# Performance work log

Hardware: AMD Instinct MI355X
Metric: run time of the kernel (lower is better)

The kernel has to match this reference:

```python
import jax, jax.numpy as jnp
import numpy as np

N = 65536      # num drones/nodes
E = 262144     # num directed edges
HID = 128      # hidden_dim
HEADS = 8      # gat1 heads
EPS = 1e-5


def _bn(x, g, b):
    # BatchNorm1d in training mode: batch statistics over dim 0 (biased var)
    mu = x.mean(0)
    var = ((x - mu) ** 2).mean(0)
    return (x - mu) * jax.lax.rsqrt(var + EPS) * g + b


def _gat(x, src, dst, W, a_src, a_dst, bias, heads, out_c, n, concat):
    # PyG GATConv math (self-loops already included in src/dst)
    xw = (x @ W).reshape(n, heads, out_c)               # [N,H,C]
    al_s = (xw * a_src).sum(-1)                          # [N,H]
    al_d = (xw * a_dst).sum(-1)                          # [N,H]
    e = jax.nn.leaky_relu(al_s[src] + al_d[dst], 0.2)    # [E',H]
    m = jax.ops.segment_max(e, dst, num_segments=n)      # stable softmax per target
    ex = jnp.exp(e - m[dst])
    den = jax.ops.segment_sum(ex, dst, num_segments=n)
    alpha = ex / den[dst]                                # [E',H]
    out = jax.ops.segment_sum(xw[src] * alpha[:, :, None], dst, num_segments=n)
    out = out.reshape(n, heads * out_c) if concat else out.mean(axis=1)
    return out + bias


def setup_inputs() -> dict:
    key = jax.random.key(0)
    ks = jax.random.split(key, 24)
    s = 0.05
    inp = {
        'node_features': jax.random.normal(ks[0], (N, HID), jnp.float32),
        'relative_poses': jax.random.normal(ks[1], (E, 6), jnp.float32),
        'pe_w1': jax.random.normal(ks[2], (6, 64), jnp.float32) * s,
        'pe_b1': jnp.zeros((64,), jnp.float32),
        'pe_g1': jnp.ones((64,), jnp.float32),
        'pe_be1': jnp.zeros((64,), jnp.float32),
        'pe_w2': jax.random.normal(ks[3], (64, HID), jnp.float32) * s,
        'pe_b2': jnp.zeros((HID,), jnp.float32),
        'pe_g2': jnp.ones((HID,), jnp.float32),
        'pe_be2': jnp.zeros((HID,), jnp.float32),
        'gamma_w': jax.random.normal(ks[4], (HID, HID), jnp.float32) * s,
        'gamma_b': jnp.zeros((HID,), jnp.float32),
        'beta_w': jax.random.normal(ks[5], (HID, HID), jnp.float32) * s,
        'beta_b': jnp.zeros((HID,), jnp.float32),
        'g1_w': jax.random.normal(ks[6], (HID, HEADS * HID), jnp.float32) * s,
        'g1_as': jax.random.normal(ks[7], (HEADS, HID), jnp.float32) * s,
        'g1_ad': jax.random.normal(ks[8], (HEADS, HID), jnp.float32) * s,
        'g1_b': jnp.zeros((HEADS * HID,), jnp.float32),
        'g2_w': jax.random.normal(ks[9], (HEADS * HID, HID), jnp.float32) * s,
        'g2_as': jax.random.normal(ks[10], (1, HID), jnp.float32) * s,
        'g2_ad': jax.random.normal(ks[11], (1, HID), jnp.float32) * s,
        'g2_b': jnp.zeros((HID,), jnp.float32),
        'edge_index': jax.random.randint(ks[12], (2, E), 0, N, jnp.int32),
    }
    return inp


def reference(node_features, relative_poses, pe_w1, pe_b1, pe_g1, pe_be1,
              pe_w2, pe_b2, pe_g2, pe_be2, gamma_w, gamma_b, beta_w, beta_b,
              g1_w, g1_as, g1_ad, g1_b, g2_w, g2_as, g2_ad, g2_b, edge_index):
    src, dst = edge_index[0], edge_index[1]
    # SpatialEncoding: pose MLP with training-mode BN, then FiLM modulation
    h = jax.nn.relu(_bn(relative_poses @ pe_w1 + pe_b1, pe_g1, pe_be1))
    h = jax.nn.relu(_bn(h @ pe_w2 + pe_b2, pe_g2, pe_be2))
    gamma = jax.nn.sigmoid(h @ gamma_w + gamma_b) * 2.0   # [E,HID]
    beta = h @ beta_w + beta_b
    modulated = gamma * node_features[src] + beta          # [E,HID]
    last = jnp.full((N,), -1, jnp.int32).at[dst].max(jnp.arange(E, dtype=jnp.int32))
    enc = jnp.where((last >= 0)[:, None], modulated[jnp.clip(last, 0)], node_features)
    # add self loops (PyG GATConv default)
    loops = jnp.arange(N, dtype=src.dtype)
    src_a = jnp.concatenate([src, loops])
    dst_a = jnp.concatenate([dst, loops])
    x = jax.nn.elu(_gat(enc, src_a, dst_a, g1_w, g1_as, g1_ad, g1_b, HEADS, HID, N, True))
    # dropout is identity in eval mode
    out = _gat(x, src_a, dst_a, g2_w, g2_as, g2_ad, g2_b, 1, HID, N, False)
    return out
```

## Files before the change

kernel.cpp:

```cpp
#include <hip/hip_runtime.h>
#include <hip/hip_bf16.h>
#include <math.h>

#define NN 65536
#define EE 262144

typedef unsigned short u16;
typedef unsigned int u32;
typedef __attribute__((ext_vector_type(8))) short bf16x8;
typedef __attribute__((ext_vector_type(4))) float f32x4;

__device__ __forceinline__ float bfu2f(u16 u){ return __uint_as_float(((u32)u)<<16); }
__device__ __forceinline__ u16 f2bfu(float f){
  u32 x = __float_as_uint(f);
  return (u16)((x + 0x7fffu + ((x>>16)&1u)) >> 16);
}
__device__ __forceinline__ float lrelu(float x){ return x>0.f ? x : 0.2f*x; }
__device__ __forceinline__ float fexp(float x){ return __expf(x); }

__global__ void k_prep(const float* __restrict__ nodef, u16* __restrict__ nodefb,
                       const float* __restrict__ pe_w2, u16* __restrict__ pe_w2t,
                       const float* __restrict__ gamma_w, u16* __restrict__ gwt,
                       const float* __restrict__ beta_w, u16* __restrict__ bwt,
                       const float* __restrict__ g1_w, u16* __restrict__ g1wt,
                       const float* __restrict__ g2_w, u16* __restrict__ g2wt,
                       const float* __restrict__ g1_as, const float* __restrict__ g1_ad,
                       u16* __restrict__ vtb,
                       const int* __restrict__ dstA, int* __restrict__ lastE, int* __restrict__ deg){
  int bid = blockIdx.x, t = threadIdx.x;
  if (bid < 8192){
    int i = (bid*256+t)*4;
    float4 v = *(const float4*)(nodef + i);
    ushort4 o; o.x=f2bfu(v.x); o.y=f2bfu(v.y); o.z=f2bfu(v.z); o.w=f2bfu(v.w);
    *(ushort4*)(nodefb + i) = o;
  } else if (bid < 8224){
    int idx = (bid-8192)*256+t;
    int k = idx>>7, n = idx&127;
    pe_w2t[n*64+k] = f2bfu(pe_w2[idx]);
  } else if (bid < 8288){
    int idx = (bid-8224)*256+t;
    int k = idx>>7, n = idx&127;
    gwt[n*128+k] = f2bfu(gamma_w[idx]);
  } else if (bid < 8352){
    int idx = (bid-8288)*256+t;
    int k = idx>>7, n = idx&127;
    bwt[n*128+k] = f2bfu(beta_w[idx]);
  } else if (bid < 8864){
    int idx = (bid-8352)*256+t;
    int k = idx>>10, n = idx&1023;
    g1wt[n*128+k] = f2bfu(g1_w[idx]);
  } else if (bid < 9376){
    int idx = (bid-8864)*256+t;
    int k = idx>>7, n = idx&127;
    g2wt[n*1024+k] = f2bfu(g2_w[idx]);
  } else if (bid < 9380){
    int gid = (bid-9376)*256+t;
    if (gid<1024){
      int h = gid>>7, k = gid&127;
      float s=0.f,d=0.f;
      for (int cc=0;cc<128;++cc){
        float wv = g1_w[(size_t)k*1024 + h*128+cc];
        s=fmaf(wv,g1_as[h*128+cc],s); d=fmaf(wv,g1_ad[h*128+cc],d);
      }
      vtb[h*128+k] = f2bfu(s);
      vtb[(h+8)*128+k] = f2bfu(d);
    }
  } else {
    int e = (bid-9380)*256+t;
    int d = dstA[e];
    atomicMax(&lastE[d], e);
    atomicAdd(&deg[d], 1);
  }
}

__launch_bounds__(256)
__global__ void k_bn1p(const float* __restrict__ poses, const float* __restrict__ w1,
                       const float* __restrict__ b1, float* __restrict__ part1){
  int t = threadIdx.x;
  int wv = t>>6, c = t&63;
  int wave = blockIdx.x*4 + wv;
  float wc[6];
#pragma unroll
  for (int j=0;j<6;++j) wc[j] = w1[j*64+c];
  float bb = b1[c];
  float s=0.f,q=0.f;
  int e0 = wave*(EE/1024);
  for (int e=e0;e<e0+(EE/1024);++e){
    float z = bb;
#pragma unroll
    for (int j=0;j<6;++j) z = fmaf(poses[e*6+j], wc[j], z);
    s += z; q += z*z;
  }
  __shared__ float ls[4][64];
  __shared__ float lq[4][64];
  ls[wv][c]=s; lq[wv][c]=q;
  __syncthreads();
  if (t<64){
    float ss = ls[0][t]+ls[1][t]+ls[2][t]+ls[3][t];
    float qq = lq[0][t]+lq[1][t]+lq[2][t]+lq[3][t];
    part1[blockIdx.x*128 + t] = ss;
    part1[blockIdx.x*128 + 64 + t] = qq;
  }
}

__global__ void k_bn_fin1(const float* __restrict__ part1,
                          const float* __restrict__ g, const float* __restrict__ be,
                          float* __restrict__ a, float* __restrict__ cc){
  int c = threadIdx.x;
  if (c<64){
    float s=0.f,q=0.f;
    for (int k=0;k<256;++k){ s += part1[k*128+c]; q += part1[k*128+64+c]; }
    float mu = s*(1.f/EE);
    float var = q*(1.f/EE) - mu*mu;
    float istd = rsqrtf(var + 1e-5f);
    float ac = istd*g[c];
    a[c] = ac;
    cc[c] = be[c] - mu*ac;
  }
}

__global__ void k_red2(const float* __restrict__ psum, const float* __restrict__ psq,
                       float* __restrict__ part2){
  int t = threadIdx.x;
  int b0 = blockIdx.x*128;
  float s = 0.f;
  if (t < 128){
    for (int k=0;k<128;++k) s += psum[(size_t)(b0+k)*128 + t];
  } else {
    int c = t-128;
    for (int k=0;k<128;++k) s += psq[(size_t)(b0+k)*128 + c];
  }
  part2[blockIdx.x*256 + t] = s;
}

__global__ void k_bn_fin2(const float* __restrict__ part2,
                          const float* __restrict__ g, const float* __restrict__ be,
                          const float* __restrict__ bias0,
                          float* __restrict__ a, float* __restrict__ cc){
  int c = threadIdx.x;
  if (c<128){
    float s=0.f,q=0.f;
    for (int k=0;k<32;++k){ s += part2[k*256+c]; q += part2[k*256+128+c]; }
    float mu = s*(1.f/EE);
    float var = q*(1.f/EE) - mu*mu;
    float istd = rsqrtf(var + 1e-5f);
    float ac = istd*g[c];
    a[c] = ac;
    cc[c] = be[c] - mu*ac + bias0[c]*ac;
  }
}

__global__ void k_h1(const float* __restrict__ poses, const float* __restrict__ w1, const float* __restrict__ b1,
                     const float* __restrict__ a1, const float* __restrict__ c1, u16* __restrict__ h1){
  int idx = blockIdx.x*256+threadIdx.x;
  int e = idx>>5, cp = (idx&31)*2;
  float z0 = b1[cp], z1 = b1[cp+1];
#pragma unroll
  for (int j=0;j<6;++j){
    float pv = poses[e*6+j];
    z0 = fmaf(pv, w1[j*64+cp], z0);
    z1 = fmaf(pv, w1[j*64+cp+1], z1);
  }
  float h0 = z0*a1[cp]+c1[cp];     h0 = h0>0.f?h0:0.f;
  float h1v = z1*a1[cp+1]+c1[cp+1]; h1v = h1v>0.f?h1v:0.f;
  *(u32*)(h1 + (size_t)e*64 + cp) = (u32)f2bfu(h0) | ((u32)f2bfu(h1v)<<16);
}

template<int EPI>
__launch_bounds__(256)
__global__ void k_mm(const u16* __restrict__ A, const u16* __restrict__ Bt,
                     const u16* __restrict__ Bt2,
                     int K, int lda, int ldbt, int ldc,
                     u16* __restrict__ outb,
                     const float* __restrict__ bias, const float* __restrict__ bias2,
                     float* __restrict__ ssum, float* __restrict__ ssq,
                     const float* __restrict__ gb,
                     const float* __restrict__ bb, const u16* __restrict__ nfselb,
                     const int* __restrict__ lastE){
  const int m0 = blockIdx.x*64, n0 = blockIdx.y*128;
  const int t = threadIdx.x;
  const int lane = t & 63, wv = t>>6;
  const int wr = wv>>1, wc = wv&1;
  __shared__ u16 Als[64*64];
  __shared__ u16 Bls[128*64];
  __shared__ u16 B2ls[EPI==7 ? 128*64 : 8];
  __shared__ float epiS[128][2];
  __shared__ float epiD[128][2];
  f32x4 acc[2][4];
  f32x4 acc2[2][4];
#pragma unroll
  for (int i=0;i<2;++i)
#pragma unroll
    for (int j=0;j<4;++j){ acc[i][j] = (f32x4){0.f,0.f,0.f,0.f}; acc2[i][j] = (f32x4){0.f,0.f,0.f,0.f}; }

  for (int k0=0;k0<K;k0+=64){
    constexpr int NS = (EPI==7) ? 10 : 6;
#pragma unroll
    for (int c=0;c<NS;++c){
      int gc = c*256 + t;
      if (gc < 512){
        int row = gc>>3, ch = gc&7;
        int sw = ((row<<3)|ch) ^ (row&7);
        *(uint4*)(Als + sw*8) = *(const uint4*)(A + (size_t)(m0+row)*lda + k0 + ch*8);
      } else if (gc < 1536){
        int g2 = gc - 512;
        int row = g2>>3, ch = g2&7;
        int sw = ((row<<3)|ch) ^ (row&7);
        *(uint4*)(Bls + sw*8) = *(const uint4*)(Bt + (size_t)(n0+row)*ldbt + k0 + ch*8);
      } else if constexpr (EPI==7){
        int g2 = gc - 1536;
        int row = g2>>3, ch = g2&7;
        int sw = ((row<<3)|ch) ^ (row&7);
        *(uint4*)(B2ls + sw*8) = *(const uint4*)(Bt2 + (size_t)(n0+row)*ldbt + k0 + ch*8);
      }
    }
    __syncthreads();
#pragma unroll
    for (int kk=0;kk<2;++kk){
      bf16x8 af[2], bfr[4];
      int ch = kk*4 + (lane>>4);
#pragma unroll
      for (int i=0;i<2;++i){
        int row = wr*32 + i*16 + (lane&15);
        int sw = ((row<<3)|ch) ^ (row&7);
        af[i] = *(const bf16x8*)(Als + sw*8);
      }
#pragma unroll
      for (int j=0;j<4;++j){
        int rowb = wc*64 + j*16 + (lane&15);
        int swb = ((rowb<<3)|ch) ^ (rowb&7);
        bfr[j] = *(const bf16x8*)(Bls + swb*8);
      }
#pragma unroll
      for (int i=0;i<2;++i)
#pragma unroll
        for (int j=0;j<4;++j)
          acc[i][j] = __builtin_amdgcn_mfma_f32_16x16x32_bf16(af[i], bfr[j], acc[i][j], 0,0,0);
      if constexpr (EPI==7){
        bf16x8 bf2[4];
#pragma unroll
        for (int j=0;j<4;++j){
          int rowb = wc*64 + j*16 + (lane&15);
          int swb = ((rowb<<3)|ch) ^ (rowb&7);
          bf2[j] = *(const bf16x8*)(B2ls + swb*8);
        }
#pragma unroll
        for (int i=0;i<2;++i)
#pragma unroll
          for (int j=0;j<4;++j)
            acc2[i][j] = __builtin_amdgcn_mfma_f32_16x16x32_bf16(af[i], bf2[j], acc2[i][j], 0,0,0);
      }
    }
    __syncthreads();
  }

  int cbase = wc*64 + (lane&15);

  if constexpr (EPI==6){
    float av[4], cv[4];
#pragma unroll
    for (int j=0;j<4;++j){ av[j]=bias[cbase+j*16]; cv[j]=bias2[cbase+j*16]; }
#pragma unroll
    for (int i=0;i<2;++i)
#pragma unroll
      for (int r=0;r<4;++r){
        int row = m0 + wr*32 + i*16 + ((lane>>4)<<2) + r;
#pragma unroll
        for (int j=0;j<4;++j){
          float h = fmaf(acc[i][j][r], av[j], cv[j]);
          outb[(size_t)row*128 + cbase + j*16] = f2bfu(h>0.f?h:0.f);
        }
      }
  } else if constexpr (EPI==2){
    float bv[4];
#pragma unroll
    for (int j=0;j<4;++j) bv[j]=bias[cbase+j*16];
    float s[4]={0,0,0,0}, q[4]={0,0,0,0};
#pragma unroll
    for (int i=0;i<2;++i)
#pragma unroll
      for (int j=0;j<4;++j)
#pragma unroll
        for (int r=0;r<4;++r){ float z = acc[i][j][r]+bv[j]; s[j]+=z; q[j]+=z*z; }
#pragma unroll
    for (int j=0;j<4;++j){
      float ss=s[j], qq=q[j];
      ss += __shfl_xor(ss,16); ss += __shfl_xor(ss,32);
      qq += __shfl_xor(qq,16); qq += __shfl_xor(qq,32);
      if (lane<16){
        epiS[wc*64+j*16+lane][wr] = ss;
        epiD[wc*64+j*16+lane][wr] = qq;
      }
    }
    __syncthreads();
    if (t<128){
      ssum[(size_t)blockIdx.x*128 + t] = epiS[t][0]+epiS[t][1];
      ssq[(size_t)blockIdx.x*128 + t]  = epiD[t][0]+epiD[t][1];
    }
  } else if constexpr (EPI==7){
    float gbv[4], bbv[4];
#pragma unroll
    for (int j=0;j<4;++j){ gbv[j]=gb[cbase+j*16]; bbv[j]=bb[cbase+j*16]; }
#pragma unroll
    for (int i=0;i<2;++i)
#pragma unroll
      for (int r=0;r<4;++r){
        int n = m0 + wr*32 + i*16 + ((lane>>4)<<2) + r;
        int le = lastE[n];
#pragma unroll
        for (int j=0;j<4;++j){
          int c = cbase + j*16;
          float nv = bfu2f(nfselb[(size_t)n*128+c]);
          float res;
          if (le>=0){
            float gp = acc[i][j][r] + gbv[j];
            float gam = 2.f/(1.f+fexp(-gp));
            res = fmaf(gam, nv, acc2[i][j][r] + bbv[j]);
          } else res = nv;
          outb[(size_t)n*128+c] = f2bfu(res);
        }
      }
  }
}

__launch_bounds__(512)
__global__ void k_proj(const u16* __restrict__ aggH, const u16* __restrict__ g1wt,
                       const u16* __restrict__ g2wt, const float* __restrict__ g1b,
                       const float* __restrict__ asv, const float* __restrict__ adv,
                       u16* __restrict__ xw2b, float* __restrict__ als2, float* __restrict__ ald2){
  const int m0 = blockIdx.x*64;
  const int t = threadIdx.x, lane = t&63, wv = t>>6;
  const int wr = wv>>1, wc = wv&1;
  __shared__ u16 ATls[64*128];
  __shared__ u16 Wls[128*64];
  __shared__ float epiS[64][2];
  __shared__ float epiD[64][2];
  const int cbase = wc*64 + (lane&15);
  f32x4 acc2[4];
#pragma unroll
  for (int j=0;j<4;++j) acc2[j] = (f32x4){0.f,0.f,0.f,0.f};

  for (int hh=0; hh<8; ++hh){
    f32x4 acc1[4];
#pragma unroll
    for (int j=0;j<4;++j) acc1[j] = (f32x4){0.f,0.f,0.f,0.f};

    for (int k0=0;k0<128;k0+=64){
#pragma unroll
      for (int c=0;c<3;++c){
        int gc = c*512 + t;
        if (gc < 512){
          int row = gc>>3, ch = gc&7;
          int sw = ((row<<3)|ch) ^ (row&7);
          *(uint4*)(ATls + sw*8) = *(const uint4*)(aggH + (size_t)(m0+row)*1024 + hh*128 + k0 + ch*8);
        } else {
          int g2 = gc - 512;
          int row = g2>>3, ch = g2&7;
          int sw = ((row<<3)|ch) ^ (row&7);
          *(uint4*)(Wls + sw*8) = *(const uint4*)(g1wt + (size_t)(hh*128+row)*128 + k0 + ch*8);
        }
      }
      __syncthreads();
      __builtin_amdgcn_s_setprio(1);
#pragma unroll
      for (int kk=0;kk<2;++kk){
        bf16x8 af, bfr[4];
        int ch = kk*4 + (lane>>4);
        {
          int row = wr*16 + (lane&15);
          int sw = ((row<<3)|ch) ^ (row&7);
          af = *(const bf16x8*)(ATls + sw*8);
        }
#pragma unroll
        for (int j=0;j<4;++j){
          int rowb = wc*64 + j*16 + (lane&15);
          int swb = ((rowb<<3)|ch) ^ (rowb&7);
          bfr[j] = *(const bf16x8*)(Wls + swb*8);
        }
#pragma unroll
        for (int j=0;j<4;++j)
          acc1[j] = __builtin_amdgcn_mfma_f32_16x16x32_bf16(af, bfr[j], acc1[j], 0,0,0);
      }
      __builtin_amdgcn_s_setprio(0);
      __syncthreads();
    }
    {
      float bv[4];
#pragma unroll
      for (int j=0;j<4;++j) bv[j] = g1b[hh*128 + cbase + j*16];
#pragma unroll
      for (int r=0;r<4;++r){
        int mrow = wr*16 + ((lane>>4)<<2) + r;
#pragma unroll
        for (int j=0;j<4;++j){
          int c = cbase + j*16;
          float v = acc1[j][r] + bv[j];
          v = v>0.f ? v : fexp(v)-1.f;
          int sw = ((mrow<<4)|(c>>3)) ^ (mrow&7);
          ATls[sw*8 + (c&7)] = f2bfu(v);
        }
      }
    }
    for (int k0=0;k0<128;k0+=64){
#pragma unroll
      for (int c=0;c<2;++c){
        int g2 = c*512 + t;
        int row = g2>>3, ch = g2&7;
        int sw = ((row<<3)|ch) ^ (row&7);
        *(uint4*)(Wls + sw*8) = *(const uint4*)(g2wt + (size_t)row*1024 + hh*128 + k0 + ch*8);
      }
      __syncthreads();
      __builtin_amdgcn_s_setprio(1);
#pragma unroll
      for (int kk=0;kk<2;++kk){
        bf16x8 af, bfr[4];
        int ch = kk*4 + (lane>>4);
        int chk = (k0>>3) + ch;
        {
          int row = wr*16 + (lane&15);
          int sw = ((row<<4)|chk) ^ (row&7);
          af = *(const bf16x8*)(ATls + sw*8);
        }
#pragma unroll
        for (int j=0;j<4;++j){
          int rowb = wc*64 + j*16 + (lane&15);
          int swb = ((rowb<<3)|ch) ^ (rowb&7);
          bfr[j] = *(const bf16x8*)(Wls + swb*8);
        }
#pragma unroll
        for (int j=0;j<4;++j)
          acc2[j] = __builtin_amdgcn_mfma_f32_16x16x32_bf16(af, bfr[j], acc2[j], 0,0,0);
      }
      __builtin_amdgcn_s_setprio(0);
      __syncthreads();
    }
  }
  float av[4], dv[4];
#pragma unroll
  for (int j=0;j<4;++j){ av[j]=asv[cbase+j*16]; dv[j]=adv[cbase+j*16]; }
#pragma unroll
  for (int r=0;r<4;++r){
    int lr = wr*16 + ((lane>>4)<<2) + r;
    int row = m0 + lr;
    float s=0.f, d=0.f;
#pragma unroll
    for (int j=0;j<4;++j){
      float v = acc2[j][r];
      xw2b[(size_t)row*128 + cbase + j*16] = f2bfu(v);
      s = fmaf(v, av[j], s); d = fmaf(v, dv[j], d);
    }
#pragma unroll
    for (int o=1;o<16;o<<=1){ s += __shfl_xor(s,o); d += __shfl_xor(d,o); }
    if ((lane&15)==0){ epiS[lr][wc]=s; epiD[lr][wc]=d; }
  }
  __syncthreads();
  if (t<64){
    als2[m0+t] = epiS[t][0]+epiS[t][1];
    ald2[m0+t] = epiD[t][0]+epiD[t][1];
  }
}

__global__ void k_blocksum(const int* __restrict__ deg, int* __restrict__ bsum){
  __shared__ int s[256];
  int t = threadIdx.x;
  s[t] = deg[blockIdx.x*256+t];
  __syncthreads();
  for (int o=128;o>0;o>>=1){ if (t<o) s[t]+=s[t+o]; __syncthreads(); }
  if (!t) bsum[blockIdx.x]=s[0];
}
__global__ void k_scanb(int* __restrict__ bsum){
  __shared__ int s[256];
  int t=threadIdx.x;
  s[t]=bsum[t]; __syncthreads();
  for (int o=1;o<256;o<<=1){
    int v = s[t];
    if (t>=o) v += s[t-o];
    __syncthreads(); s[t]=v; __syncthreads();
  }
  bsum[t] = t ? s[t-1] : 0;
}
__global__ void k_indptr(const int* __restrict__ deg, const int* __restrict__ bsum, int* __restrict__ indptr){
  __shared__ int s[256];
  int t=threadIdx.x; int g=blockIdx.x*256+t;
  int d = deg[g];
  s[t]=d; __syncthreads();
  for (int o=1;o<256;o<<=1){
    int v = s[t];
    if (t>=o) v += s[t-o];
    __syncthreads(); s[t]=v; __syncthreads();
  }
  indptr[g] = bsum[blockIdx.x] + s[t] - d;
  if (g==NN-1) indptr[NN]=EE;
}
__global__ void k_fill(const int* __restrict__ srcA, const int* __restrict__ dstA,
                       const int* __restrict__ indptr, int* __restrict__ cursor, int* __restrict__ slist){
  int e = blockIdx.x*256+threadIdx.x;
  int d = dstA[e];
  int p = atomicAdd(&cursor[d],1);
  slist[indptr[d]+p] = srcA[e];
}

__global__ void k_gsel(const u16* __restrict__ h1, const u16* __restrict__ nodefb,
                       const int* __restrict__ lastE, const int* __restrict__ srcA,
                       u16* __restrict__ h1sel, u16* __restrict__ nfselb){
  int g = blockIdx.x*256+threadIdx.x;
  int n = g>>4, ch = g&15;
  int le = lastE[n];
  int src = (le>=0) ? srcA[le] : n;
  *(uint4*)(nfselb + (size_t)n*128 + ch*8) = *(const uint4*)(nodefb + (size_t)src*128 + ch*8);
  if (ch < 8){
    uint4 v = make_uint4(0,0,0,0);
    if (le>=0) v = *(const uint4*)(h1 + (size_t)le*64 + ch*8);
    *(uint4*)(h1sel + (size_t)n*64 + ch*8) = v;
  }
}

__launch_bounds__(256)
__global__ void k_als1mm(const u16* __restrict__ encb, const u16* __restrict__ vtb,
                         float* __restrict__ als, float* __restrict__ ald){
  int t = threadIdx.x, lane = t&63, wv = t>>6;
  int m0 = blockIdx.x*64 + wv*16;
  f32x4 acc = (f32x4){0.f,0.f,0.f,0.f};
  const u16* arow = encb + (size_t)(m0 + (lane&15))*128;
  const u16* brow = vtb + (lane&15)*128;
  int ko = (lane>>4)*8;
#pragma unroll
  for (int k0=0;k0<128;k0+=32){
    bf16x8 af = *(const bf16x8*)(arow + k0 + ko);
    bf16x8 bf = *(const bf16x8*)(brow + k0 + ko);
    acc = __builtin_amdgcn_mfma_f32_16x16x32_bf16(af, bf, acc, 0,0,0);
  }
  int o = lane&15;
#pragma unroll
  for (int r=0;r<4;++r){
    int row = m0 + ((lane>>4)<<2) + r;
    if (o<8) als[(size_t)row*8+o] = acc[r];
    else     ald[(size_t)row*8+(o-8)] = acc[r];
  }
}

__launch_bounds__(256)
__global__ void k_soft1(const int* __restrict__ slist, const int* __restrict__ indptr,
                        const float* __restrict__ als, const float* __restrict__ ald,
                        float* __restrict__ wcsr, float* __restrict__ den1, float* __restrict__ wself1){
  int t = threadIdx.x;
  int n = blockIdx.x*4 + (t>>6);
  int lane = t&63;
  int ei = lane>>3, h = lane&7;
  int p0 = indptr[n], p1 = indptr[n+1];
  float adh = ald[(size_t)n*8+h];
  float selfsc = lrelu(als[(size_t)n*8+h] + adh);
  float m = selfsc;
  for (int p=p0+ei; p<p1; p+=8){
    int s = slist[p];
    m = fmaxf(m, lrelu(als[(size_t)s*8+h] + adh));
  }
  m = fmaxf(m, __shfl_xor(m,8));
  m = fmaxf(m, __shfl_xor(m,16));
  m = fmaxf(m, __shfl_xor(m,32));
  float ws = fexp(selfsc - m);
  float den = (ei==0) ? ws : 0.f;
  for (int p=p0+ei; p<p1; p+=8){
    int s = slist[p];
    float w = fexp(lrelu(als[(size_t)s*8+h] + adh) - m);
    wcsr[(size_t)p*8+h] = w;
    den += w;
  }
  den += __shfl_xor(den,8);
  den += __shfl_xor(den,16);
  den += __shfl_xor(den,32);
  if (ei==0){
    den1[(size_t)n*8+h] = den;
    wself1[(size_t)n*8+h] = ws;
  }
}

__launch_bounds__(256)
__global__ void k_soft2(const int* __restrict__ slist, const int* __restrict__ indptr,
                        const float* __restrict__ als, const float* __restrict__ ald,
                        float* __restrict__ wcsr, float* __restrict__ den2, float* __restrict__ wself2){
  int t = threadIdx.x;
  int n = blockIdx.x*16 + (t>>4);
  int l = t&15;
  int p0 = indptr[n], p1 = indptr[n+1];
  float adh = ald[n];
  float selfsc = lrelu(als[n] + adh);
  float m = selfsc;
  for (int p=p0+l; p<p1; p+=16)
    m = fmaxf(m, lrelu(als[slist[p]] + adh));
  m = fmaxf(m, __shfl_xor(m,1));
  m = fmaxf(m, __shfl_xor(m,2));
  m = fmaxf(m, __shfl_xor(m,4));
  m = fmaxf(m, __shfl_xor(m,8));
  float ws = fexp(selfsc - m);
  float den = (l==0) ? ws : 0.f;
  for (int p=p0+l; p<p1; p+=16){
    float w = fexp(lrelu(als[slist[p]] + adh) - m);
    wcsr[p] = w;
    den += w;
  }
  den += __shfl_xor(den,1);
  den += __shfl_xor(den,2);
  den += __shfl_xor(den,4);
  den += __shfl_xor(den,8);
  if (l==0){ den2[n] = den; wself2[n] = ws; }
}

__launch_bounds__(256)
__global__ void k_agg1(const u16* __restrict__ encb, const float* __restrict__ wcsr,
                       const float* __restrict__ den1, const float* __restrict__ wself1,
                       const int* __restrict__ slist, const int* __restrict__ indptr,
                       u16* __restrict__ aggH){
  int t = threadIdx.x;
  int n = blockIdx.x*4 + (t>>6);
  int lane = t&63;
  int c0 = lane*2;
  int p0 = indptr[n], p1 = indptr[n+1];
  float a0[8], a1[8];
  {
    ushort2 u = *(const ushort2*)(encb + (size_t)n*128 + c0);
    float x0 = bfu2f(u.x), x1 = bfu2f(u.y);
#pragma unroll
    for (int h=0;h<8;++h){
      float ws = wself1[(size_t)n*8 + h];
      a0[h] = ws*x0; a1[h] = ws*x1;
    }
  }
  for (int p=p0; p<p1; ++p){
    int s = slist[p];
    float4 w0 = *(const float4*)(wcsr + (size_t)p*8);
    float4 w1 = *(const float4*)(wcsr + (size_t)p*8 + 4);
    ushort2 u = *(const ushort2*)(encb + (size_t)s*128 + c0);
    float x0 = bfu2f(u.x), x1 = bfu2f(u.y);
    a0[0]=fmaf(w0.x,x0,a0[0]); a1[0]=fmaf(w0.x,x1,a1[0]);
    a0[1]=fmaf(w0.y,x0,a0[1]); a1[1]=fmaf(w0.y,x1,a1[1]);
    a0[2]=fmaf(w0.z,x0,a0[2]); a1[2]=fmaf(w0.z,x1,a1[2]);
    a0[3]=fmaf(w0.w,x0,a0[3]); a1[3]=fmaf(w0.w,x1,a1[3]);
    a0[4]=fmaf(w1.x,x0,a0[4]); a1[4]=fmaf(w1.x,x1,a1[4]);
    a0[5]=fmaf(w1.y,x0,a0[5]); a1[5]=fmaf(w1.y,x1,a1[5]);
    a0[6]=fmaf(w1.z,x0,a0[6]); a1[6]=fmaf(w1.z,x1,a1[6]);
    a0[7]=fmaf(w1.w,x0,a0[7]); a1[7]=fmaf(w1.w,x1,a1[7]);
  }
#pragma unroll
  for (int h=0;h<8;++h){
    float rr = 1.f/den1[(size_t)n*8 + h];
    u32 pk = (u32)f2bfu(a0[h]*rr) | ((u32)f2bfu(a1[h]*rr)<<16);
    *(u32*)(aggH + (size_t)n*1024 + h*128 + c0) = pk;
  }
}

__launch_bounds__(256)
__global__ void k_gat2(const u16* __restrict__ xw2b, const float* __restrict__ wcsr,
                       const float* __restrict__ den2, const float* __restrict__ wself2,
                       const int* __restrict__ slist, const int* __restrict__ indptr,
                       const float* __restrict__ g2b, float* __restrict__ out){
  int t = threadIdx.x;
  int n = blockIdx.x*4 + (t>>6);
  int c0 = (t&63)*2;
  int p0 = indptr[n], p1 = indptr[n+1];
  float ws = wself2[n];
  u32 u = *(const u32*)(xw2b + (size_t)n*128 + c0);
  float a0 = ws*bfu2f((u16)u), a1 = ws*bfu2f((u16)(u>>16));
  int p = p0;
  for (; p+2<=p1; p+=2){
    int s0=slist[p], s1=slist[p+1];
    float w0=wcsr[p], w1v=wcsr[p+1];
    u32 v0 = *(const u32*)(xw2b + (size_t)s0*128 + c0);
    u32 v1 = *(const u32*)(xw2b + (size_t)s1*128 + c0);
    a0 = fmaf(w0, bfu2f((u16)v0), a0);       a1 = fmaf(w0, bfu2f((u16)(v0>>16)), a1);
    a0 = fmaf(w1v, bfu2f((u16)v1), a0);      a1 = fmaf(w1v, bfu2f((u16)(v1>>16)), a1);
  }
  for (; p<p1; ++p){
    int s = slist[p];
    float w = wcsr[p];
    u32 v = *(const u32*)(xw2b + (size_t)s*128 + c0);
    a0 = fmaf(w, bfu2f((u16)v), a0);
    a1 = fmaf(w, bfu2f((u16)(v>>16)), a1);
  }
  float rr = 1.f/den2[n];
  float2 o;
  o.x = a0*rr + g2b[c0];
  o.y = a1*rr + g2b[c0+1];
  *(float2*)(out + (size_t)n*128 + c0) = o;
}

extern "C" void kernel_launch(void* const* d_in, const int* in_sizes, int n_in,
                              void* d_out, int out_size, void* d_ws, size_t ws_size,
                              hipStream_t stream){
  const float* nodef  = (const float*)d_in[0];
  const float* poses  = (const float*)d_in[1];
  const float* pe_w1  = (const float*)d_in[2];
  const float* pe_b1  = (const float*)d_in[3];
  const float* pe_g1  = (const float*)d_in[4];
  const float* pe_be1 = (const float*)d_in[5];
  const float* pe_w2  = (const float*)d_in[6];
  const float* pe_b2  = (const float*)d_in[7];
  const float* pe_g2  = (const float*)d_in[8];
  const float* pe_be2 = (const float*)d_in[9];
  const float* gamma_w= (const float*)d_in[10];
  const float* gamma_b= (const float*)d_in[11];
  const float* beta_w = (const float*)d_in[12];
  const float* beta_b = (const float*)d_in[13];
  const float* g1_w   = (const float*)d_in[14];
  const float* g1_as  = (const float*)d_in[15];
  const float* g1_ad  = (const float*)d_in[16];
  const float* g1_b   = (const float*)d_in[17];
  const float* g2_w   = (const float*)d_in[18];
  const float* g2_as  = (const float*)d_in[19];
  const float* g2_ad  = (const float*)d_in[20];
  const float* g2_b   = (const float*)d_in[21];
  const int*   eidx   = (const int*)d_in[22];
  const int* srcA = eidx;
  const int* dstA = eidx + EE;

  char* w = (char*)d_ws;
  const size_t MB = 1048576;
  u16*   aggH  = (u16*)(w + 0);
  u16*   h1    = (u16*)(w + 0);
  u16*   h1sel = (u16*)(w + 32*MB);
  u16*   h2b   = (u16*)(w + 40*MB);
  u16*   nodefb= (u16*)(w + 56*MB);
  u16*   nfselb= (u16*)(w + 72*MB);
  float* psum  = (float*)(w + 88*MB);
  float* psq   = (float*)(w + 90*MB);
  u16*   encb  = (u16*)(w + 128*MB);
  char* sm = w + 144*MB;
  size_t off = 0;
  auto alloc = [&](size_t b)->void*{ void* p = sm+off; off += (b+255)&~(size_t)255; return p; };
  u16* pe_w2t = (u16*)alloc(64*128*2);
  u16* gwt    = (u16*)alloc(128*128*2);
  u16* bwt    = (u16*)alloc(128*128*2);
  u16* g1wt   = (u16*)alloc(1024*128*2);
  u16* g2wt   = (u16*)alloc(128*1024*2);
  u16* vtb    = (u16*)alloc(16*128*2);
  float* part2 = (float*)alloc(32*256*4);
  float* part1 = (float*)alloc(256*128*4);
  float* als1  = (float*)alloc((size_t)NN*8*4);
  float* ald1  = (float*)alloc((size_t)NN*8*4);
  float* als2  = (float*)alloc((size_t)NN*4);
  float* ald2  = (float*)alloc((size_t)NN*4);
  float* wself1= (float*)alloc((size_t)NN*8*4);
  float* den1  = (float*)alloc((size_t)NN*8*4);
  float* wcsr1 = (float*)alloc((size_t)EE*8*4);
  float* wself2= (float*)alloc((size_t)NN*4);
  float* den2  = (float*)alloc((size_t)NN*4);
  float* wcsr2 = (float*)alloc((size_t)EE*4);
  u16*  xw2b   = (u16*)alloc((size_t)NN*128*2);
  int* lastE   = (int*)alloc((size_t)NN*4);
  int* deg     = (int*)alloc((size_t)NN*4);
  int* cursor  = (int*)alloc((size_t)NN*4);
  int* indptr  = (int*)alloc((size_t)(NN+1)*4);
  int* slist   = (int*)alloc((size_t)EE*4);
  int* bsum    = (int*)alloc(1024);
  float* stats = (float*)alloc(4096);
  float* a1 = stats+384, *c1 = stats+448, *a2 = stats+512, *c2 = stats+640;

  hipMemsetAsync(deg, 0, (size_t)NN*4, stream);
  hipMemsetAsync(cursor, 0, (size_t)NN*4, stream);
  hipMemsetAsync(lastE, 0xFF, (size_t)NN*4, stream);

  k_prep<<<10404,256,0,stream>>>(nodef, nodefb, pe_w2, pe_w2t, gamma_w, gwt, beta_w, bwt,
                                 g1_w, g1wt, g2_w, g2wt, g1_as, g1_ad, vtb,
                                 dstA, lastE, deg);

  k_bn1p<<<256,256,0,stream>>>(poses, pe_w1, pe_b1, part1);
  k_bn_fin1<<<1,64,0,stream>>>(part1, pe_g1, pe_be1, a1, c1);
  k_h1<<<32768,256,0,stream>>>(poses, pe_w1, pe_b1, a1, c1, h1);

  k_mm<2><<<dim3(4096,1),256,0,stream>>>(h1, pe_w2t, nullptr, 64, 64, 64, 0,
      nullptr, pe_b2, nullptr, psum, psq, nullptr, nullptr, nullptr, nullptr);
  k_red2<<<32,256,0,stream>>>(psum, psq, part2);
  k_bn_fin2<<<1,128,0,stream>>>(part2, pe_g2, pe_be2, pe_b2, a2, c2);

  k_blocksum<<<256,256,0,stream>>>(deg, bsum);
  k_scanb<<<1,256,0,stream>>>(bsum);
  k_indptr<<<256,256,0,stream>>>(deg, bsum, indptr);
  k_fill<<<1024,256,0,stream>>>(srcA, dstA, indptr, cursor, slist);

  k_gsel<<<4096,256,0,stream>>>(h1, nodefb, lastE, srcA, h1sel, nfselb);
  k_mm<6><<<dim3(1024,1),256,0,stream>>>(h1sel, pe_w2t, nullptr, 64, 64, 64, 128,
      h2b, a2, c2, nullptr, nullptr, nullptr, nullptr, nullptr, nullptr);

  k_mm<7><<<dim3(1024,1),256,0,stream>>>(h2b, gwt, bwt, 128, 128, 128, 128,
      encb, nullptr, nullptr, nullptr, nullptr, gamma_b, beta_b, nfselb, lastE);

  k_als1mm<<<1024,256,0,stream>>>(encb, vtb, als1, ald1);
  k_soft1<<<NN/4,256,0,stream>>>(slist, indptr, als1, ald1, wcsr1, den1, wself1);

  k_agg1<<<NN/4,256,0,stream>>>(encb, wcsr1, den1, wself1, slist, indptr, aggH);

  k_proj<<<1024,512,0,stream>>>(aggH, g1wt, g2wt, g1_b, g2_as, g2_ad, xw2b, als2, ald2);

  k_soft2<<<NN/16,256,0,stream>>>(slist, indptr, als2, ald2, wcsr2, den2, wself2);
  k_gat2<<<NN/4,256,0,stream>>>(xw2b, wcsr2, den2, wself2, slist, indptr, g2_b, (float*)d_out);
}
```

Baseline: 420.9 us.

## Fuse GAT softmax into aggregation kernels, recomputing edge weights in place

Drops the separate softmax kernels for both GAT layers. The aggregation kernels now compute the per-target max, the exp weights and the denominator themselves, reading attention logits straight from the source nodes. This removes the per-edge weight arrays (EE*8 and EE floats), their write and read-back, and two launches. In exchange every lane redundantly computes all heads' exps, and the max pass is serial per node rather than spread across lanes.

Result: slower. 464.6 us (+10.4%).

```diff
diff --git a/kernel.cpp b/kernel.cpp
--- a/kernel.cpp
+++ b/kernel.cpp
@@ -540,144 +540,91 @@
 }
 
 __launch_bounds__(256)
-__global__ void k_soft1(const int* __restrict__ slist, const int* __restrict__ indptr,
+__global__ void k_fagg1(const u16* __restrict__ encb,
                         const float* __restrict__ als, const float* __restrict__ ald,
-                        float* __restrict__ wcsr, float* __restrict__ den1, float* __restrict__ wself1){
-  int t = threadIdx.x;
-  int n = blockIdx.x*4 + (t>>6);
-  int lane = t&63;
-  int ei = lane>>3, h = lane&7;
-  int p0 = indptr[n], p1 = indptr[n+1];
-  float adh = ald[(size_t)n*8+h];
-  float selfsc = lrelu(als[(size_t)n*8+h] + adh);
-  float m = selfsc;
-  for (int p=p0+ei; p<p1; p+=8){
-    int s = slist[p];
-    m = fmaxf(m, lrelu(als[(size_t)s*8+h] + adh));
-  }
-  m = fmaxf(m, __shfl_xor(m,8));
-  m = fmaxf(m, __shfl_xor(m,16));
-  m = fmaxf(m, __shfl_xor(m,32));
-  float ws = fexp(selfsc - m);
-  float den = (ei==0) ? ws : 0.f;
-  for (int p=p0+ei; p<p1; p+=8){
-    int s = slist[p];
-    float w = fexp(lrelu(als[(size_t)s*8+h] + adh) - m);
-    wcsr[(size_t)p*8+h] = w;
-    den += w;
-  }
-  den += __shfl_xor(den,8);
-  den += __shfl_xor(den,16);
-  den += __shfl_xor(den,32);
-  if (ei==0){
-    den1[(size_t)n*8+h] = den;
-    wself1[(size_t)n*8+h] = ws;
-  }
-}
-
-__launch_bounds__(256)
-__global__ void k_soft2(const int* __restrict__ slist, const int* __restrict__ indptr,
-                        const float* __restrict__ als, const float* __restrict__ ald,
-                        float* __restrict__ wcsr, float* __restrict__ den2, float* __restrict__ wself2){
-  int t = threadIdx.x;
-  int n = blockIdx.x*16 + (t>>4);
-  int l = t&15;
-  int p0 = indptr[n], p1 = indptr[n+1];
-  float adh = ald[n];
-  float selfsc = lrelu(als[n] + adh);
-  float m = selfsc;
-  for (int p=p0+l; p<p1; p+=16)
-    m = fmaxf(m, lrelu(als[slist[p]] + adh));
-  m = fmaxf(m, __shfl_xor(m,1));
-  m = fmaxf(m, __shfl_xor(m,2));
-  m = fmaxf(m, __shfl_xor(m,4));
-  m = fmaxf(m, __shfl_xor(m,8));
-  float ws = fexp(selfsc - m);
-  float den = (l==0) ? ws : 0.f;
-  for (int p=p0+l; p<p1; p+=16){
-    float w = fexp(lrelu(als[slist[p]] + adh) - m);
-    wcsr[p] = w;
-    den += w;
-  }
-  den += __shfl_xor(den,1);
-  den += __shfl_xor(den,2);
-  den += __shfl_xor(den,4);
-  den += __shfl_xor(den,8);
-  if (l==0){ den2[n] = den; wself2[n] = ws; }
-}
-
-__launch_bounds__(256)
-__global__ void k_agg1(const u16* __restrict__ encb, const float* __restrict__ wcsr,
-                       const float* __restrict__ den1, const float* __restrict__ wself1,
-                       const int* __restrict__ slist, const int* __restrict__ indptr,
-                       u16* __restrict__ aggH){
+                        const int* __restrict__ slist, const int* __restrict__ indptr,
+                        u16* __restrict__ aggH){
   int t = threadIdx.x;
   int n = blockIdx.x*4 + (t>>6);
   int lane = t&63;
   int c0 = lane*2;
   int p0 = indptr[n], p1 = indptr[n+1];
-  float a0[8], a1[8];
+  float adh[8], selfsc[8], m[8];
+#pragma unroll
+  for (int h=0;h<8;++h){
+    adh[h] = ald[(size_t)n*8+h];
+    selfsc[h] = lrelu(als[(size_t)n*8+h] + adh[h]);
+    m[h] = selfsc[h];
+  }
+  for (int p=p0; p<p1; ++p){
+    int s = slist[p];
+    float4 v0 = *(const float4*)(als + (size_t)s*8);
+    float4 v1 = *(const float4*)(als + (size_t)s*8 + 4);
+    m[0]=fmaxf(m[0],lrelu(v0.x+adh[0])); m[1]=fmaxf(m[1],lrelu(v0.y+adh[1]));
+    m[2]=fmaxf(m[2],lrelu(v0.z+adh[2])); m[3]=fmaxf(m[3],lrelu(v0.w+adh[3]));
+    m[4]=fmaxf(m[4],lrelu(v1.x+adh[4])); m[5]=fmaxf(m[5],lrelu(v1.y+adh[5]));
+    m[6]=fmaxf(m[6],lrelu(v1.z+adh[6])); m[7]=fmaxf(m[7],lrelu(v1.w+adh[7]));
+  }
+  float a0[8], a1[8], den[8];
   {
     ushort2 u = *(const ushort2*)(encb + (size_t)n*128 + c0);
     float x0 = bfu2f(u.x), x1 = bfu2f(u.y);
 #pragma unroll
     for (int h=0;h<8;++h){
-      float ws = wself1[(size_t)n*8 + h];
-      a0[h] = ws*x0; a1[h] = ws*x1;
+      float ws = fexp(selfsc[h] - m[h]);
+      den[h] = ws; a0[h] = ws*x0; a1[h] = ws*x1;
     }
   }
   for (int p=p0; p<p1; ++p){
     int s = slist[p];
-    float4 w0 = *(const float4*)(wcsr + (size_t)p*8);
-    float4 w1 = *(const float4*)(wcsr + (size_t)p*8 + 4);
+    float4 v0 = *(const float4*)(als + (size_t)s*8);
+    float4 v1 = *(const float4*)(als + (size_t)s*8 + 4);
     ushort2 u = *(const ushort2*)(encb + (size_t)s*128 + c0);
     float x0 = bfu2f(u.x), x1 = bfu2f(u.y);
-    a0[0]=fmaf(w0.x,x0,a0[0]); a1[0]=fmaf(w0.x,x1,a1[0]);
-    a0[1]=fmaf(w0.y,x0,a0[1]); a1[1]=fmaf(w0.y,x1,a1[1]);
-    a0[2]=fmaf(w0.z,x0,a0[2]); a1[2]=fmaf(w0.z,x1,a1[2]);
-    a0[3]=fmaf(w0.w,x0,a0[3]); a1[3]=fmaf(w0.w,x1,a1[3]);
-    a0[4]=fmaf(w1.x,x0,a0[4]); a1[4]=fmaf(w1.x,x1,a1[4]);
-    a0[5]=fmaf(w1.y,x0,a0[5]); a1[5]=fmaf(w1.y,x1,a1[5]);
-    a0[6]=fmaf(w1.z,x0,a0[6]); a1[6]=fmaf(w1.z,x1,a1[6]);
-    a0[7]=fmaf(w1.w,x0,a0[7]); a1[7]=fmaf(w1.w,x1,a1[7]);
+    float w0 = fexp(lrelu(v0.x+adh[0])-m[0]); den[0]+=w0; a0[0]=fmaf(w0,x0,a0[0]); a1[0]=fmaf(w0,x1,a1[0]);
+    float w1 = fexp(lrelu(v0.y+adh[1])-m[1]); den[1]+=w1; a0[1]=fmaf(w1,x0,a0[1]); a1[1]=fmaf(w1,x1,a1[1]);
+    float w2 = fexp(lrelu(v0.z+adh[2])-m[2]); den[2]+=w2; a0[2]=fmaf(w2,x0,a0[2]); a1[2]=fmaf(w2,x1,a1[2]);
+    float w3 = fexp(lrelu(v0.w+adh[3])-m[3]); den[3]+=w3; a0[3]=fmaf(w3,x0,a0[3]); a1[3]=fmaf(w3,x1,a1[3]);
+    float w4 = fexp(lrelu(v1.x+adh[4])-m[4]); den[4]+=w4; a0[4]=fmaf(w4,x0,a0[4]); a1[4]=fmaf(w4,x1,a1[4]);
+    float w5 = fexp(lrelu(v1.y+adh[5])-m[5]); den[5]+=w5; a0[5]=fmaf(w5,x0,a0[5]); a1[5]=fmaf(w5,x1,a1[5]);
+    float w6 = fexp(lrelu(v1.z+adh[6])-m[6]); den[6]+=w6; a0[6]=fmaf(w6,x0,a0[6]); a1[6]=fmaf(w6,x1,a1[6]);
+    float w7 = fexp(lrelu(v1.w+adh[7])-m[7]); den[7]+=w7; a0[7]=fmaf(w7,x0,a0[7]); a1[7]=fmaf(w7,x1,a1[7]);
   }
 #pragma unroll
   for (int h=0;h<8;++h){
-    float rr = 1.f/den1[(size_t)n*8 + h];
+    float rr = 1.f/den[h];
     u32 pk = (u32)f2bfu(a0[h]*rr) | ((u32)f2bfu(a1[h]*rr)<<16);
     *(u32*)(aggH + (size_t)n*1024 + h*128 + c0) = pk;
   }
 }
 
 __launch_bounds__(256)
-__global__ void k_gat2(const u16* __restrict__ xw2b, const float* __restrict__ wcsr,
-                       const float* __restrict__ den2, const float* __restrict__ wself2,
-                       const int* __restrict__ slist, const int* __restrict__ indptr,
-                       const float* __restrict__ g2b, float* __restrict__ out){
+__global__ void k_fgat2(const u16* __restrict__ xw2b,
+                        const float* __restrict__ als, const float* __restrict__ ald,
+                        const int* __restrict__ slist, const int* __restrict__ indptr,
+                        const float* __restrict__ g2b, float* __restrict__ out){
   int t = threadIdx.x;
   int n = blockIdx.x*4 + (t>>6);
   int c0 = (t&63)*2;
   int p0 = indptr[n], p1 = indptr[n+1];
-  float ws = wself2[n];
+  float adh = ald[n];
+  float selfsc = lrelu(als[n] + adh);
+  float m = selfsc;
+  for (int p=p0; p<p1; ++p)
+    m = fmaxf(m, lrelu(als[slist[p]] + adh));
   u32 u = *(const u32*)(xw2b + (size_t)n*128 + c0);
+  float ws = fexp(selfsc - m);
+  float den = ws;
   float a0 = ws*bfu2f((u16)u), a1 = ws*bfu2f((u16)(u>>16));
-  int p = p0;
-  for (; p+2<=p1; p+=2){
-    int s0=slist[p], s1=slist[p+1];
-    float w0=wcsr[p], w1v=wcsr[p+1];
-    u32 v0 = *(const u32*)(xw2b + (size_t)s0*128 + c0);
-    u32 v1 = *(const u32*)(xw2b + (size_t)s1*128 + c0);
-    a0 = fmaf(w0, bfu2f((u16)v0), a0);       a1 = fmaf(w0, bfu2f((u16)(v0>>16)), a1);
-    a0 = fmaf(w1v, bfu2f((u16)v1), a0);      a1 = fmaf(w1v, bfu2f((u16)(v1>>16)), a1);
-  }
-  for (; p<p1; ++p){
+  for (int p=p0; p<p1; ++p){
     int s = slist[p];
-    float w = wcsr[p];
+    float w = fexp(lrelu(als[s] + adh) - m);
     u32 v = *(const u32*)(xw2b + (size_t)s*128 + c0);
+    den += w;
     a0 = fmaf(w, bfu2f((u16)v), a0);
     a1 = fmaf(w, bfu2f((u16)(v>>16)), a1);
   }
-  float rr = 1.f/den2[n];
+  float rr = 1.f/den;
   float2 o;
   o.x = a0*rr + g2b[c0];
   o.y = a1*rr + g2b[c0+1];
@@ -739,12 +686,6 @@
   float* ald1  = (float*)alloc((size_t)NN*8*4);
   float* als2  = (float*)alloc((size_t)NN*4);
   float* ald2  = (float*)alloc((size_t)NN*4);
-  float* wself1= (float*)alloc((size_t)NN*8*4);
-  float* den1  = (float*)alloc((size_t)NN*8*4);
-  float* wcsr1 = (float*)alloc((size_t)EE*8*4);
-  float* wself2= (float*)alloc((size_t)NN*4);
-  float* den2  = (float*)alloc((size_t)NN*4);
-  float* wcsr2 = (float*)alloc((size_t)EE*4);
   u16*  xw2b   = (u16*)alloc((size_t)NN*128*2);
   int* lastE   = (int*)alloc((size_t)NN*4);
   int* deg     = (int*)alloc((size_t)NN*4);
@@ -785,12 +726,9 @@
       encb, nullptr, nullptr, nullptr, nullptr, gamma_b, beta_b, nfselb, lastE);
 
   k_als1mm<<<1024,256,0,stream>>>(encb, vtb, als1, ald1);
-  k_soft1<<<NN/4,256,0,stream>>>(slist, indptr, als1, ald1, wcsr1, den1, wself1);
-
-  k_agg1<<<NN/4,256,0,stream>>>(encb, wcsr1, den1, wself1, slist, indptr, aggH);
+  k_fagg1<<<NN/4,256,0,stream>>>(encb, als1, ald1, slist, indptr, aggH);
 
   k_proj<<<1024,512,0,stream>>>(aggH, g1wt, g2wt, g1_b, g2_as, g2_ad, xw2b, als2, ald2);
 
-  k_soft2<<<NN/16,256,0,stream>>>(slist, indptr, als2, ald2, wcsr2, den2, wself2);
-  k_gat2<<<NN/4,256,0,stream>>>(xw2b, wcsr2, den2, wself2, slist, indptr, g2_b, (float*)d_out);
-}
+  k_fgat2<<<NN/4,256,0,stream>>>(xw2b, als2, ald2, slist, indptr, g2_b, (float*)d_out);
+}
```
